# Kernel tuning notes

Measured on AMD Instinct MI355X. Metric: run time of the kernel, lower is better.

## Reference

```python
import jax, jax.numpy as jnp
import numpy as np

B = 131072

def _grid_P():
    # P[k] = ((i-6)/6, (j-6)/6, 1) with k = 13*i + j
    ii, jj = jnp.meshgrid(jnp.arange(13), jnp.arange(13), indexing='ij')
    P = jnp.stack([(ii - 6) / 6.0, (jj - 6) / 6.0, jnp.ones_like(ii)], axis=-1)
    return P.reshape(169, 3).astype(jnp.float32)  # [169,3], shared across batch

def setup_inputs() -> dict:
    key = jax.random.key(0)
    k0, k1, k2, k3, k4 = jax.random.split(key, 5)
    return {
        'eyes': jax.random.normal(k0, (B, 3), dtype=jnp.float32),
        'v': jax.random.normal(k1, (B, 3), dtype=jnp.float32),
        'R': jax.random.normal(k2, (B, 3, 3), dtype=jnp.float32),
        't': jax.random.normal(k3, (B, 3), dtype=jnp.float32),
        'alpha': jax.random.uniform(k4, (B,), dtype=jnp.float32),
    }

def reference(eyes, v, R, t, alpha):
    P = _grid_P()  # [169,3]
    # normalize gaze direction (clamped L2 norm, as in torch)
    vn = v / jnp.clip(jnp.linalg.norm(v, axis=1, keepdims=True), 1e-14, None)
    # M = v v^T - alpha * I   [B,3,3]
    M = vn[:, :, None] * vn[:, None, :] - alpha[:, None, None] * jnp.eye(3, dtype=v.dtype)
    # rows of the projection basis: v1 = R[:,:,0], v2 = R[:,:,1], t - eyes
    W = jnp.stack([R[:, :, 0], R[:, :, 1], t - eyes], axis=1)  # [B,3,3]
    # sigma[b,a,c] = W[b,a,:] @ M[b] @ W[b,c,:]
    sigma = jnp.einsum('bai,bij,bcj->bac', W, M, W)  # [B,3,3]
    # quadratic form per grid point: out[b,k] = P[k] @ sigma[b] @ P[k]
    out = jnp.einsum('ki,bij,kj->bk', P, sigma, P)  # [B,169]
    return out
```

## Files before the change

kernel.cpp:

```cpp
#include <hip/hip_runtime.h>

#define BLK 256
#define NB  8
#define NV4 ((NB * 169) / 4)

typedef float v4f __attribute__((ext_vector_type(4)));

__global__ __launch_bounds__(BLK) void cone_fused_kernel(
    const float* __restrict__ eyes,
    const float* __restrict__ v,
    const float* __restrict__ R,
    const float* __restrict__ t,
    const float* __restrict__ alpha,
    float* __restrict__ out,
    int B, int total4)
{
    __shared__ float c[NB][6];
    const int tid = threadIdx.x;
    const int b0  = blockIdx.x * NB;

    if (tid < NB) {
        const int b = b0 + tid;
        if (b < B) {
            float vx = v[b*3+0], vy = v[b*3+1], vz = v[b*3+2];
            float n  = sqrtf(vx*vx + vy*vy + vz*vz);
            n = fmaxf(n, 1e-14f);
            const float inv = 1.0f / n;
            vx *= inv; vy *= inv; vz *= inv;
            const float a = alpha[b];

            const float* Rb = R + (size_t)b * 9;
            const float w0x = Rb[0], w0y = Rb[3], w0z = Rb[6];
            const float w1x = Rb[1], w1y = Rb[4], w1z = Rb[7];
            const float w2x = t[b*3+0] - eyes[b*3+0];
            const float w2y = t[b*3+1] - eyes[b*3+1];
            const float w2z = t[b*3+2] - eyes[b*3+2];

            const float d0 = vx*w0x + vy*w0y + vz*w0z;
            const float d1 = vx*w1x + vy*w1y + vz*w1z;
            const float d2 = vx*w2x + vy*w2y + vz*w2z;

            c[tid][0] = d0*d0 - a*(w0x*w0x + w0y*w0y + w0z*w0z);
            c[tid][1] = d1*d1 - a*(w1x*w1x + w1y*w1y + w1z*w1z);
            c[tid][2] = d2*d2 - a*(w2x*w2x + w2y*w2y + w2z*w2z);
            c[tid][3] = 2.0f * (d0*d1 - a*(w0x*w1x + w0y*w1y + w0z*w1z));
            c[tid][4] = 2.0f * (d0*d2 - a*(w0x*w2x + w0y*w2y + w0z*w2z));
            c[tid][5] = 2.0f * (d1*d2 - a*(w1x*w2x + w1y*w2y + w1z*w2z));
        }
    }
    __syncthreads();

    const size_t base4 = (size_t)blockIdx.x * NV4;
    #pragma unroll
    for (int r = 0; r < 2; ++r) {
        const int idx = tid + r * BLK;
        if (idx < NV4 && (int)(base4 + idx) < total4) {
            const int lf = idx * 4;
            int bl = (lf * 388) >> 16;
            int k  = lf - 169 * bl;

            float s00 = c[bl][0], s11 = c[bl][1], s22 = c[bl][2];
            float t01 = c[bl][3], t02 = c[bl][4], t12 = c[bl][5];

            v4f rv;
            #pragma unroll
            for (int e = 0; e < 4; ++e) {
                if (k == 169) {
                    ++bl; k = 0;
                    s00 = c[bl][0]; s11 = c[bl][1]; s22 = c[bl][2];
                    t01 = c[bl][3]; t02 = c[bl][4]; t12 = c[bl][5];
                }
                const int iq = (k * 20165) >> 18;
                const int j  = k - 13 * iq;
                const float px = (float)(iq - 6) * (1.0f / 6.0f);
                const float py = (float)(j  - 6) * (1.0f / 6.0f);
                rv[e] = s22 + px * (s00 * px + t01 * py + t02)
                            + py * (s11 * py + t12);
                ++k;
            }
            __builtin_nontemporal_store(rv, (v4f*)out + base4 + idx);
        }
    }
}

extern "C" void kernel_launch(void* const* d_in, const int* in_sizes, int n_in,
                              void* d_out, int out_size, void* d_ws, size_t ws_size,
                              hipStream_t stream) {
    const float* eyes  = (const float*)d_in[0];
    const float* v     = (const float*)d_in[1];
    const float* R     = (const float*)d_in[2];
    const float* t     = (const float*)d_in[3];
    const float* alpha = (const float*)d_in[4];
    float* out = (float*)d_out;

    const int B = in_sizes[4];
    const int total4 = out_size / 4;
    const int grid = (B + NB - 1) / NB;

    cone_fused_kernel<<<grid, BLK, 0, stream>>>(eyes, v, R, t, alpha, out, B, total4);
}
```

Before: 120.9 us.

## Compute one batch row per thread and process 256 rows per block

Each block now handles 256 batch elements, with every thread computing one element's six quadratic-form coefficients instead of only 8 threads doing setup work. Coefficients are stored as two float4 values in shared memory and loaded with vector reads, and the row-crossing branch in the inner loop becomes branchless selects between two preloaded coefficient sets. The goal is less per-block setup overhead, better input-load parallelism and less divergence. In exchange there are far fewer blocks, each running a longer store loop, and the next-row float4 read may touch an unwritten padding slot.

New measurement: 113.7 us. 6.0% less time.

```diff
diff --git a/kernel.cpp b/kernel.cpp
--- a/kernel.cpp
+++ b/kernel.cpp
@@ -1,8 +1,9 @@
 #include <hip/hip_runtime.h>
 
 #define BLK 256
-#define NB  8
+#define NB  256
 #define NV4 ((NB * 169) / 4)
+#define NIT ((NV4 + BLK - 1) / BLK)
 
 typedef float v4f __attribute__((ext_vector_type(4)));
 
@@ -15,68 +16,75 @@
     float* __restrict__ out,
     int B, int total4)
 {
-    __shared__ float c[NB][6];
+    __shared__ v4f c4[2 * (NB + 1)];
     const int tid = threadIdx.x;
     const int b0  = blockIdx.x * NB;
+    const int b   = b0 + tid;
 
-    if (tid < NB) {
-        const int b = b0 + tid;
-        if (b < B) {
-            float vx = v[b*3+0], vy = v[b*3+1], vz = v[b*3+2];
-            float n  = sqrtf(vx*vx + vy*vy + vz*vz);
-            n = fmaxf(n, 1e-14f);
-            const float inv = 1.0f / n;
-            vx *= inv; vy *= inv; vz *= inv;
-            const float a = alpha[b];
+    if (b < B) {
+        float vx = v[b*3+0], vy = v[b*3+1], vz = v[b*3+2];
+        float n  = sqrtf(vx*vx + vy*vy + vz*vz);
+        n = fmaxf(n, 1e-14f);
+        const float inv = 1.0f / n;
+        vx *= inv; vy *= inv; vz *= inv;
+        const float a = alpha[b];
 
-            const float* Rb = R + (size_t)b * 9;
-            const float w0x = Rb[0], w0y = Rb[3], w0z = Rb[6];
-            const float w1x = Rb[1], w1y = Rb[4], w1z = Rb[7];
-            const float w2x = t[b*3+0] - eyes[b*3+0];
-            const float w2y = t[b*3+1] - eyes[b*3+1];
-            const float w2z = t[b*3+2] - eyes[b*3+2];
+        const float* Rb = R + (size_t)b * 9;
+        const float w0x = Rb[0], w0y = Rb[3], w0z = Rb[6];
+        const float w1x = Rb[1], w1y = Rb[4], w1z = Rb[7];
+        const float w2x = t[b*3+0] - eyes[b*3+0];
+        const float w2y = t[b*3+1] - eyes[b*3+1];
+        const float w2z = t[b*3+2] - eyes[b*3+2];
 
-            const float d0 = vx*w0x + vy*w0y + vz*w0z;
-            const float d1 = vx*w1x + vy*w1y + vz*w1z;
-            const float d2 = vx*w2x + vy*w2y + vz*w2z;
+        const float d0 = vx*w0x + vy*w0y + vz*w0z;
+        const float d1 = vx*w1x + vy*w1y + vz*w1z;
+        const float d2 = vx*w2x + vy*w2y + vz*w2z;
 
-            c[tid][0] = d0*d0 - a*(w0x*w0x + w0y*w0y + w0z*w0z);
-            c[tid][1] = d1*d1 - a*(w1x*w1x + w1y*w1y + w1z*w1z);
-            c[tid][2] = d2*d2 - a*(w2x*w2x + w2y*w2y + w2z*w2z);
-            c[tid][3] = 2.0f * (d0*d1 - a*(w0x*w1x + w0y*w1y + w0z*w1z));
-            c[tid][4] = 2.0f * (d0*d2 - a*(w0x*w2x + w0y*w2y + w0z*w2z));
-            c[tid][5] = 2.0f * (d1*d2 - a*(w1x*w2x + w1y*w2y + w1z*w2z));
-        }
+        const float s00 = d0*d0 - a*(w0x*w0x + w0y*w0y + w0z*w0z);
+        const float s11 = d1*d1 - a*(w1x*w1x + w1y*w1y + w1z*w1z);
+        const float s22 = d2*d2 - a*(w2x*w2x + w2y*w2y + w2z*w2z);
+        const float t01 = 2.0f * (d0*d1 - a*(w0x*w1x + w0y*w1y + w0z*w1z));
+        const float t02 = 2.0f * (d0*d2 - a*(w0x*w2x + w0y*w2y + w0z*w2z));
+        const float t12 = 2.0f * (d1*d2 - a*(w1x*w2x + w1y*w2y + w1z*w2z));
+
+        v4f lo = {s00, s11, s22, t01};
+        v4f hi = {t02, t12, 0.0f, 0.0f};
+        c4[2*tid+0] = lo;
+        c4[2*tid+1] = hi;
     }
     __syncthreads();
 
     const size_t base4 = (size_t)blockIdx.x * NV4;
-    #pragma unroll
-    for (int r = 0; r < 2; ++r) {
-        const int idx = tid + r * BLK;
+    for (int it = 0; it < NIT; ++it) {
+        const int idx = it * BLK + tid;
         if (idx < NV4 && (int)(base4 + idx) < total4) {
-            const int lf = idx * 4;
-            int bl = (lf * 388) >> 16;
-            int k  = lf - 169 * bl;
+            const int lfl = idx * 4;
+            int row = (int)(((unsigned long long)lfl * 1626496491ULL) >> 38);
+            int k0  = lfl - 169 * row;
 
-            float s00 = c[bl][0], s11 = c[bl][1], s22 = c[bl][2];
-            float t01 = c[bl][3], t02 = c[bl][4], t12 = c[bl][5];
+            const v4f alo = c4[2*row+0];
+            const v4f ahi = c4[2*row+1];
+            const v4f blo = c4[2*row+2];
+            const v4f bhi = c4[2*row+3];
 
             v4f rv;
             #pragma unroll
             for (int e = 0; e < 4; ++e) {
-                if (k == 169) {
-                    ++bl; k = 0;
-                    s00 = c[bl][0]; s11 = c[bl][1]; s22 = c[bl][2];
-                    t01 = c[bl][3]; t02 = c[bl][4]; t12 = c[bl][5];
-                }
+                const int kk  = k0 + e;
+                const bool nx = (kk >= 169);
+                const int k   = nx ? kk - 169 : kk;
+                const float s00 = nx ? blo.x : alo.x;
+                const float s11 = nx ? blo.y : alo.y;
+                const float s22 = nx ? blo.z : alo.z;
+                const float t01 = nx ? blo.w : alo.w;
+                const float t02 = nx ? bhi.x : ahi.x;
+                const float t12 = nx ? bhi.y : ahi.y;
                 const int iq = (k * 20165) >> 18;
                 const int j  = k - 13 * iq;
                 const float px = (float)(iq - 6) * (1.0f / 6.0f);
                 const float py = (float)(j  - 6) * (1.0f / 6.0f);
                 rv[e] = s22 + px * (s00 * px + t01 * py + t02)
                             + py * (s11 * py + t12);
-                ++k;
             }
             __builtin_nontemporal_store(rv, (v4f*)out + base4 + idx);
         }
```
